# Performance work log

Measured on AMD Instinct MI355X. Metric: run time of the kernel, lower is better.

## Reference

```python
import jax, jax.numpy as jnp
import numpy as np

B, C, D, H, W = 4, 256, 16, 16, 16
REDUCTION = 8
CR = C // REDUCTION  # q/k channel dim = 32


def setup_inputs() -> dict:
    key = jax.random.key(0)
    k1, k2, k3, k4, k5, k6 = jax.random.split(key, 6)
    x = jax.random.normal(k1, (B, C, D, H, W), dtype=jnp.float32)
    # 1x1x1 conv weights are just [out_ch, in_ch] matrices
    Wq = jax.random.normal(k2, (CR, C), dtype=jnp.float32) * (1.0 / np.sqrt(C))
    Wk = jax.random.normal(k3, (CR, C), dtype=jnp.float32) * (1.0 / np.sqrt(C))
    Wv = jax.random.normal(k4, (C, C), dtype=jnp.float32) * (1.0 / np.sqrt(C))
    Wo = jax.random.normal(k5, (C, C), dtype=jnp.float32) * (1.0 / np.sqrt(C))
    gamma = jnp.zeros((1,), dtype=jnp.float32) + 0.5  # nonzero so output depends on attention
    return {"x": x, "Wq": Wq, "Wk": Wk, "Wv": Wv, "Wo": Wo, "gamma": gamma}


def reference(x, Wq, Wk, Wv, Wo, gamma):
    b, c, d, h, w = x.shape
    n = d * h * w
    scale = Wq.shape[0] ** -0.5  # (channels // reduction) ** -0.5
    xf = x.reshape(b, c, n)                      # [B, C, N]
    q = jnp.einsum('oc,bcn->bon', Wq, xf)        # [B, CR, N]
    k = jnp.einsum('oc,bcn->bon', Wk, xf)        # [B, CR, N]
    v = jnp.einsum('oc,bcn->bon', Wv, xf)        # [B, C, N]
    attn = jax.nn.softmax(jnp.einsum('bcn,bcm->bnm', q, k) * scale, axis=-1)  # [B, N, N]
    out = jnp.einsum('bcm,bnm->bcn', v, attn)    # v @ attn^T -> [B, C, N]
    out = jnp.einsum('oc,bcn->bon', Wo, out)     # output 1x1x1 conv
    out = out.reshape(b, c, d, h, w)
    return gamma[0] * out + x
```

## Files before the change

### kernel.cpp

```cpp
#include <hip/hip_runtime.h>
#include <hip/hip_bf16.h>

#define BATCH 4
#define CH 256
#define CRD 32
#define NN 4096

typedef __bf16 bf16x8 __attribute__((ext_vector_type(8)));
typedef float floatx4 __attribute__((ext_vector_type(4)));
typedef float floatx16 __attribute__((ext_vector_type(16)));
typedef unsigned short ushort4v __attribute__((ext_vector_type(4)));
typedef unsigned short ushort8v __attribute__((ext_vector_type(8)));
typedef unsigned int uint2v __attribute__((ext_vector_type(2)));
typedef unsigned int uint4v __attribute__((ext_vector_type(4)));

static __device__ __forceinline__ unsigned short f2bf(float f) {
    __bf16 h = (__bf16)f;
    return __builtin_bit_cast(unsigned short, h);
}
static __device__ __forceinline__ float bf2f(unsigned short h) {
    return __uint_as_float((unsigned int)h << 16);
}


__global__ __launch_bounds__(256) void wconv_kernel(
    const float* __restrict__ Wq, const float* __restrict__ Wk,
    const float* __restrict__ Wv, const float* __restrict__ Wo,
    unsigned short* __restrict__ What, unsigned short* __restrict__ WobF)
{
    const int o = blockIdx.x;
    const int t = threadIdx.x;
    float scale = 1.0f;
    const float* src;
    if (o < 32)      { src = Wq + o * 256;
                       scale = 0.17677669529663687f * 1.4426950408889634f; }
    else if (o < 64) { src = Wk + (o - 32) * 256; }
    else             { src = Wv + (o - 64) * 256; }
    const int mb = o >> 5;
    const size_t idx = ((size_t)(mb * 16 + (t >> 4)) * 64
                        + (o & 31) + 32 * ((t >> 3) & 1)) * 8 + (t & 7);
    What[idx] = f2bf(src[t] * scale);
    if (o < 256) {
        const size_t i2 = ((size_t)((o >> 5) * 16 + (t >> 4)) * 64
                           + (o & 31) + 32 * ((t >> 3) & 1)) * 8 + (t & 7);
        WobF[i2] = f2bf(Wo[o * 256 + t]);
    }
}

static __device__ __forceinline__ uint4v hmerge(
    const ushort4v& xp, const ushort4v& yp, int h)
{
    uint2v xd = __builtin_bit_cast(uint2v, xp);
    uint2v yd = __builtin_bit_cast(uint2v, yp);
    unsigned int px0 = (unsigned int)__shfl_xor((int)xd[0], 32);
    unsigned int px1 = (unsigned int)__shfl_xor((int)xd[1], 32);
    unsigned int py0 = (unsigned int)__shfl_xor((int)yd[0], 32);
    unsigned int py1 = (unsigned int)__shfl_xor((int)yd[1], 32);
    uint4v st;
    st[0] = h ? py0 : xd[0];
    st[1] = h ? py1 : xd[1];
    st[2] = h ? yd[0] : px0;
    st[3] = h ? yd[1] : px1;
    return st;
}

__global__ __launch_bounds__(256, 2) void qkv_kernel(
    const float* __restrict__ x, const unsigned short* __restrict__ What,
    unsigned short* __restrict__ qh, unsigned short* __restrict__ kh,
    unsigned short* __restrict__ vh)
{
    __shared__ __align__(16) unsigned short xf[16 * 512];

    const int t = threadIdx.x;
    const int w = t >> 6;
    const int l = t & 63;
    const int l31 = l & 31;
    const int h = l >> 5;
    const int nt = blockIdx.x, b = blockIdx.y;
    const int n0 = nt * 32;

    {
        const float* xb = x + (size_t)(b * CH) * NN + n0;
        const int n = t & 31;
        const int cq = t >> 5;
        #pragma unroll
        for (int p = 0; p < 8; ++p) {
            int c = p * 32 + cq * 4;
            float v0 = xb[(size_t)(c + 0) * NN + n];
            float v1 = xb[(size_t)(c + 1) * NN + n];
            float v2 = xb[(size_t)(c + 2) * NN + n];
            float v3 = xb[(size_t)(c + 3) * NN + n];
            ushort4v u4;
            u4[0] = f2bf(v0); u4[1] = f2bf(v1); u4[2] = f2bf(v2); u4[3] = f2bf(v3);
            int addr = ((2 * p + (cq >> 2)) * 64 + n + 32 * ((cq >> 1) & 1)) * 8
                       + 4 * (cq & 1);
            *(ushort4v*)&xf[addr] = u4;
        }
    }
    __syncthreads();

    const int mb0 = w, mb1 = w + 4, mb2 = w + 8;
    floatx16 acc0, acc1, acc2;
    #pragma unroll
    for (int i = 0; i < 16; ++i) { acc0[i] = 0.f; acc1[i] = 0.f; acc2[i] = 0.f; }

    for (int kblk = 0; kblk < 16; ++kblk) {
        bf16x8 bf = *(const bf16x8*)&xf[kblk * 512 + l * 8];
        bf16x8 a0 = *(const bf16x8*)(What + ((size_t)(mb0 * 16 + kblk) * 64 + l) * 8);
        bf16x8 a1 = *(const bf16x8*)(What + ((size_t)(mb1 * 16 + kblk) * 64 + l) * 8);
        acc0 = __builtin_amdgcn_mfma_f32_32x32x16_bf16(a0, bf, acc0, 0, 0, 0);
        acc1 = __builtin_amdgcn_mfma_f32_32x32x16_bf16(a1, bf, acc1, 0, 0, 0);
        if (w < 2) {
            bf16x8 a2 = *(const bf16x8*)(What + ((size_t)(mb2 * 16 + kblk) * 64 + l) * 8);
            acc2 = __builtin_amdgcn_mfma_f32_32x32x16_bf16(a2, bf, acc2, 0, 0, 0);
        }
    }

    auto store_qk = [&](unsigned short* dst, const floatx16& a) {
        size_t base = (size_t)(b * 128 + nt) * 1024;
        #pragma unroll
        for (int sb = 0; sb < 2; ++sb) {
            ushort4v xp, yp;
            #pragma unroll
            for (int i = 0; i < 4; ++i) {
                xp[i] = f2bf(a[8 * sb + i]);
                yp[i] = f2bf(a[8 * sb + 4 + i]);
            }
            uint4v st = hmerge(xp, yp, h);
            *(uint4v*)(dst + base + (size_t)sb * 512 + (size_t)l * 8) = st;
        }
    };

    if (w == 0)      store_qk(qh, acc0);
    else if (w == 1) store_qk(kh, acc0);

    __syncthreads();

    auto store_v_lds = [&](int cblk, const floatx16& a) {
        const int chunk = cblk * 2 + (l31 >> 4);
        const int hib = (l31 >> 3) & 1;
        #pragma unroll
        for (int r = 0; r < 16; ++r) {
            int rowo = (r & 3) + 8 * (r >> 2) + 4 * h;
            int unit = chunk * 64 + hib * 32 + rowo;
            int pu = unit ^ ((unit >> 5) & 7);
            xf[pu * 8 + (l31 & 7)] = f2bf(a[r]);
        }
    };

    if (w >= 2) store_v_lds(w - 2, acc0);
    store_v_lds(w + 2, acc1);
    if (w < 2) store_v_lds(w + 6, acc2);

    __syncthreads();

    #pragma unroll
    for (int p = 0; p < 4; ++p) {
        int Lu = p * 256 + t;
        int pu = Lu ^ ((Lu >> 5) & 7);
        uint4v d = *(const uint4v*)&xf[pu * 8];
        int chunk = Lu >> 6;
        int cblk = chunk >> 1, sub = chunk & 1;
        size_t dst = (((size_t)b * 8 + cblk) * 256 + nt * 2 + sub) * 512
                     + (size_t)(Lu & 63) * 8;
        *(uint4v*)(vh + dst) = d;
    }
}

#define SM_M0 12.0f

__global__ __launch_bounds__(256, 4) void attn_kernel(
    const unsigned short* __restrict__ qh, const unsigned short* __restrict__ kh,
    const unsigned short* __restrict__ vh, unsigned short* __restrict__ Opart,
    float* __restrict__ ml)
{
    __shared__ unsigned short p_lds[2 * 8 * 64 * 8];
    __shared__ float psum_s[4][32];

    const int t = threadIdx.x;
    const int w = t >> 6;
    const int l = t & 63;
    const int l31 = l & 31;
    const int h = l >> 5;

    const int lin = blockIdx.x + ((int)blockIdx.y << 7) + ((int)blockIdx.z << 9);
    const int slot = lin >> 3;
    const int combo = ((lin & 7) << 1) | (slot >> 7);
    const int g  = slot & 127;
    const int ks = combo & 3;
    const int b  = combo >> 2;

    const unsigned short* qB = qh + (size_t)(b * 128 + g) * 1024;
    const unsigned short* kB = kh + (size_t)b * 128 * 1024;
    const unsigned short* vB = vh + (size_t)b * 8 * 256 * 512;

    bf16x8 qf0 = *(const bf16x8*)(qB + l * 8);
    bf16x8 qf1 = *(const bf16x8*)(qB + 512 + l * 8);

    bf16x8 kf0 = *(const bf16x8*)(kB + (size_t)(ks * 32 + w) * 1024 + l * 8);
    bf16x8 kf1 = *(const bf16x8*)(kB + (size_t)(ks * 32 + w) * 1024 + 512 + l * 8);

    float l_loc = 0.f;
    floatx16 acc0, acc1;
    #pragma unroll
    for (int i = 0; i < 16; ++i) { acc0[i] = 0.f; acc1[i] = 0.f; }

    for (int it = 0; it < 8; ++it) {
        const int pbase = (it & 1) << 12;

        floatx16 sacc;
        #pragma unroll
        for (int i = 0; i < 16; ++i) sacc[i] = 0.f;
        __builtin_amdgcn_s_setprio(1);
        sacc = __builtin_amdgcn_mfma_f32_32x32x16_bf16(kf0, qf0, sacc, 0, 0, 0);
        sacc = __builtin_amdgcn_mfma_f32_32x32x16_bf16(kf1, qf1, sacc, 0, 0, 0);
        __builtin_amdgcn_s_setprio(0);

        float pv[16];
        #pragma unroll
        for (int r = 0; r < 16; ++r) pv[r] = __builtin_exp2f(sacc[r] - SM_M0);
        float s0 = (pv[0] + pv[1]) + (pv[2] + pv[3]);
        float s1 = (pv[4] + pv[5]) + (pv[6] + pv[7]);
        float s2 = (pv[8] + pv[9]) + (pv[10] + pv[11]);
        float s3 = (pv[12] + pv[13]) + (pv[14] + pv[15]);
        l_loc += (s0 + s1) + (s2 + s3);
        #pragma unroll
        for (int rg = 0; rg < 4; ++rg) {
            ushort4v pk;
            #pragma unroll
            for (int i = 0; i < 4; ++i) pk[i] = f2bf(pv[rg * 4 + i]);
            int idx = pbase
                    + ((2 * w + (rg >> 1)) * 64 + l31 + 32 * (rg & 1)) * 8 + 4 * h;
            *(ushort4v*)&p_lds[idx] = pk;
        }
        if (it < 7) {
            const unsigned short* kn = kB + (size_t)(ks * 32 + (it + 1) * 4 + w) * 1024;
            kf0 = *(const bf16x8*)(kn + l * 8);
            kf1 = *(const bf16x8*)(kn + 512 + l * 8);
        }
        const unsigned short* v0b = vB + ((size_t)(2 * w) * 256 + (ks * 8 + it) * 8) * 512;
        const unsigned short* v1b = vB + ((size_t)(2 * w + 1) * 256 + (ks * 8 + it) * 8) * 512;
        bf16x8 va = *(const bf16x8*)(v0b + l * 8);
        bf16x8 vc = *(const bf16x8*)(v1b + l * 8);

        __syncthreads();

        bf16x8 pf = *(const bf16x8*)&p_lds[pbase + l * 8];
        #pragma unroll
        for (int s = 0; s < 8; ++s) {
            bf16x8 va_n, vc_n, pf_n;
            if (s < 7) {
                va_n = *(const bf16x8*)(v0b + (s + 1) * 512 + l * 8);
                vc_n = *(const bf16x8*)(v1b + (s + 1) * 512 + l * 8);
                pf_n = *(const bf16x8*)&p_lds[pbase + ((s + 1) * 64 + l) * 8];
            }
            __builtin_amdgcn_s_setprio(1);
            acc0 = __builtin_amdgcn_mfma_f32_32x32x16_bf16(va, pf, acc0, 0, 0, 0);
            acc1 = __builtin_amdgcn_mfma_f32_32x32x16_bf16(vc, pf, acc1, 0, 0, 0);
            __builtin_amdgcn_s_setprio(0);
            va = va_n; vc = vc_n; pf = pf_n;
        }
    }

    float lt = l_loc + __shfl_xor(l_loc, 32);
    if (h == 0) psum_s[w][l31] = lt;
    __syncthreads();
    float l_run = (psum_s[0][l31] + psum_s[1][l31])
                + (psum_s[2][l31] + psum_s[3][l31]);

    unsigned short* op = Opart + ((size_t)((b * 128 + g) * 4 + ks)) * 8192;
    #pragma unroll
    for (int ct = 0; ct < 2; ++ct) {
        const floatx16& a = ct ? acc1 : acc0;
        #pragma unroll
        for (int sb = 0; sb < 2; ++sb) {
            ushort4v xp, yp;
            #pragma unroll
            for (int i = 0; i < 4; ++i) {
                xp[i] = f2bf(a[8 * sb + i]);
                yp[i] = f2bf(a[8 * sb + 4 + i]);
            }
            uint4v st = hmerge(xp, yp, h);
            int sP = 4 * w + 2 * ct + sb;
            *(uint4v*)(op + ((size_t)sP * 64 + l) * 8) = st;
        }
    }
    if (w == 0 && h == 0) {
        size_t mb = ((size_t)(b * 128 + g) * 4 + ks) * 64;
        ml[mb + l31] = SM_M0;
        ml[mb + 32 + l31] = l_run;
    }
}

__global__ __launch_bounds__(256, 2) void out_kernel(
    const unsigned short* __restrict__ Opart, const float* __restrict__ ml,
    const unsigned short* __restrict__ WobF, const float* __restrict__ x,
    const float* __restrict__ gamma, float* __restrict__ out)
{
    const int t = threadIdx.x;
    const int w = t >> 6;
    const int l = t & 63;
    const int l31 = l & 31;
    const int h = l >> 5;
    const int qt = blockIdx.x, b = blockIdx.y;

    const size_t slot = (size_t)(b * 128 + qt) * 4;
    float m0 = ml[(slot + 0) * 64 + l31], l0 = ml[(slot + 0) * 64 + 32 + l31];
    float m1 = ml[(slot + 1) * 64 + l31], l1 = ml[(slot + 1) * 64 + 32 + l31];
    float m2 = ml[(slot + 2) * 64 + l31], l2 = ml[(slot + 2) * 64 + 32 + l31];
    float m3 = ml[(slot + 3) * 64 + l31], l3 = ml[(slot + 3) * 64 + 32 + l31];
    float M = fmaxf(fmaxf(m0, m1), fmaxf(m2, m3));
    float e0 = __builtin_exp2f(m0 - M), e1 = __builtin_exp2f(m1 - M);
    float e2 = __builtin_exp2f(m2 - M), e3 = __builtin_exp2f(m3 - M);
    float Lc = l0 * e0 + l1 * e1 + l2 * e2 + l3 * e3;
    float rL = 1.0f / Lc;
    float w0 = e0 * rL, w1 = e1 * rL, w2 = e2 * rL, w3 = e3 * rL;

    const unsigned short* o0 = Opart + (slot + 0) * 8192;
    const unsigned short* o1 = Opart + (slot + 1) * 8192;
    const unsigned short* o2 = Opart + (slot + 2) * 8192;
    const unsigned short* o3 = Opart + (slot + 3) * 8192;

    floatx16 acc[2];
    #pragma unroll
    for (int m = 0; m < 2; ++m)
        #pragma unroll
        for (int i = 0; i < 16; ++i) acc[m][i] = 0.f;

    for (int s = 0; s < 16; ++s) {
        ushort8v f0 = *(const ushort8v*)(o0 + (s * 64 + l) * 8);
        ushort8v f1 = *(const ushort8v*)(o1 + (s * 64 + l) * 8);
        ushort8v f2 = *(const ushort8v*)(o2 + (s * 64 + l) * 8);
        ushort8v f3 = *(const ushort8v*)(o3 + (s * 64 + l) * 8);
        ushort8v cmb;
        #pragma unroll
        for (int j = 0; j < 8; ++j)
            cmb[j] = f2bf(w0 * bf2f(f0[j]) + w1 * bf2f(f1[j])
                        + w2 * bf2f(f2[j]) + w3 * bf2f(f3[j]));
        bf16x8 bfr = *(bf16x8*)&cmb;
        #pragma unroll
        for (int m = 0; m < 2; ++m) {
            int mt = 2 * w + m;
            bf16x8 af = *(const bf16x8*)(WobF + ((size_t)(mt * 16 + s) * 64 + l) * 8);
            acc[m] = __builtin_amdgcn_mfma_f32_32x32x16_bf16(af, bfr, acc[m], 0, 0, 0);
        }
    }

    const float gm = gamma[0];
    #pragma unroll
    for (int m = 0; m < 2; ++m)
        #pragma unroll
        for (int r = 0; r < 16; ++r) {
            int o = (2 * w + m) * 32 + (r & 3) + 8 * (r >> 2) + 4 * h;
            int n = qt * 32 + l31;
            size_t oi = ((size_t)(b * 256 + o)) * NN + n;
            out[oi] = gm * acc[m][r] + x[oi];
        }
}

extern "C" void kernel_launch(void* const* d_in, const int* in_sizes, int n_in,
                              void* d_out, int out_size, void* d_ws, size_t ws_size,
                              hipStream_t stream)
{
    const float* x     = (const float*)d_in[0];
    const float* Wq    = (const float*)d_in[1];
    const float* Wk    = (const float*)d_in[2];
    const float* Wv    = (const float*)d_in[3];
    const float* Wo    = (const float*)d_in[4];
    const float* gamma = (const float*)d_in[5];
    float* out = (float*)d_out;

    char* wsb = (char*)d_ws;
    unsigned short* qh    = (unsigned short*)(wsb);
    unsigned short* kh    = (unsigned short*)(wsb + (1u << 20));
    unsigned short* vh    = (unsigned short*)(wsb + (2u << 20));
    unsigned short* What  = (unsigned short*)(wsb + (10u << 20));
    unsigned short* WobF  = (unsigned short*)(wsb + (10u << 20) + (256u << 10));
    unsigned short* Opart = (unsigned short*)(wsb + (11u << 20));
    float*          ml    = (float*)         (wsb + (45u << 20));

    wconv_kernel<<<320, 256, 0, stream>>>(Wq, Wk, Wv, Wo, What, WobF);

    dim3 g1(128, BATCH);
    qkv_kernel<<<g1, 256, 0, stream>>>(x, What, qh, kh, vh);

    dim3 g2(128, 4, BATCH);
    attn_kernel<<<g2, 256, 0, stream>>>(qh, kh, vh, Opart, ml);

    dim3 g3(128, BATCH);
    out_kernel<<<g3, 256, 0, stream>>>(Opart, ml, WobF, x, gamma, out);
}
```

Baseline: 153.7 us.

## Process two query tiles per attention block to share V loads across tiles

The attention kernel now uses 512 threads per block and covers two 32-row query tiles in each block. Each wave owns a 32-channel slice of V, loads its eight V fragments once, and applies them to the P tiles of both query groups. This halves the number of blocks and the global V traffic per query tile. In exchange, V register pressure per wave rises, LDS use doubles, and the grid shrinks to 1024 blocks, which may reduce latency hiding.

```diff
diff --git a/kernel.cpp b/kernel.cpp
--- a/kernel.cpp
+++ b/kernel.cpp
@@ -169,44 +169,47 @@
 
 #define SM_M0 12.0f
 
-__global__ __launch_bounds__(256, 4) void attn_kernel(
+__global__ __launch_bounds__(512, 4) void attn_kernel(
     const unsigned short* __restrict__ qh, const unsigned short* __restrict__ kh,
     const unsigned short* __restrict__ vh, unsigned short* __restrict__ Opart,
     float* __restrict__ ml)
 {
-    __shared__ unsigned short p_lds[2 * 8 * 64 * 8];
-    __shared__ float psum_s[4][32];
+    __shared__ unsigned short p_lds[2 * 16 * 64 * 8];
+    __shared__ float psum_s[8][32];
 
     const int t = threadIdx.x;
     const int w = t >> 6;
     const int l = t & 63;
     const int l31 = l & 31;
     const int h = l >> 5;
-
-    const int lin = blockIdx.x + ((int)blockIdx.y << 7) + ((int)blockIdx.z << 9);
+    const int wk = w & 3;
+    const int hq = w >> 2;
+
+    const int lin = blockIdx.x + ((int)blockIdx.y << 6) + ((int)blockIdx.z << 8);
     const int slot = lin >> 3;
-    const int combo = ((lin & 7) << 1) | (slot >> 7);
-    const int g  = slot & 127;
+    const int combo = ((lin & 7) << 1) | (slot >> 6);
+    const int gp = slot & 63;
     const int ks = combo & 3;
     const int b  = combo >> 2;
-
-    const unsigned short* qB = qh + (size_t)(b * 128 + g) * 1024;
+    const int g0 = 2 * gp, g1 = 2 * gp + 1;
+
+    const unsigned short* qB = qh + (size_t)(b * 128 + (hq ? g1 : g0)) * 1024;
     const unsigned short* kB = kh + (size_t)b * 128 * 1024;
     const unsigned short* vB = vh + (size_t)b * 8 * 256 * 512;
 
     bf16x8 qf0 = *(const bf16x8*)(qB + l * 8);
     bf16x8 qf1 = *(const bf16x8*)(qB + 512 + l * 8);
 
-    bf16x8 kf0 = *(const bf16x8*)(kB + (size_t)(ks * 32 + w) * 1024 + l * 8);
-    bf16x8 kf1 = *(const bf16x8*)(kB + (size_t)(ks * 32 + w) * 1024 + 512 + l * 8);
+    bf16x8 kf0 = *(const bf16x8*)(kB + (size_t)(ks * 32 + wk) * 1024 + l * 8);
+    bf16x8 kf1 = *(const bf16x8*)(kB + (size_t)(ks * 32 + wk) * 1024 + 512 + l * 8);
 
     float l_loc = 0.f;
-    floatx16 acc0, acc1;
-    #pragma unroll
-    for (int i = 0; i < 16; ++i) { acc0[i] = 0.f; acc1[i] = 0.f; }
+    floatx16 acc_a, acc_b;
+    #pragma unroll
+    for (int i = 0; i < 16; ++i) { acc_a[i] = 0.f; acc_b[i] = 0.f; }
 
     for (int it = 0; it < 8; ++it) {
-        const int pbase = (it & 1) << 12;
+        const int pbase = (it & 1) << 13;
 
         floatx16 sacc;
         #pragma unroll
@@ -230,48 +233,72 @@
             #pragma unroll
             for (int i = 0; i < 4; ++i) pk[i] = f2bf(pv[rg * 4 + i]);
             int idx = pbase
-                    + ((2 * w + (rg >> 1)) * 64 + l31 + 32 * (rg & 1)) * 8 + 4 * h;
+                    + ((hq * 8 + 2 * wk + (rg >> 1)) * 64
+                       + l31 + 32 * (rg & 1)) * 8 + 4 * h;
             *(ushort4v*)&p_lds[idx] = pk;
         }
         if (it < 7) {
-            const unsigned short* kn = kB + (size_t)(ks * 32 + (it + 1) * 4 + w) * 1024;
+            const unsigned short* kn = kB + (size_t)(ks * 32 + (it + 1) * 4 + wk) * 1024;
             kf0 = *(const bf16x8*)(kn + l * 8);
             kf1 = *(const bf16x8*)(kn + 512 + l * 8);
         }
-        const unsigned short* v0b = vB + ((size_t)(2 * w) * 256 + (ks * 8 + it) * 8) * 512;
-        const unsigned short* v1b = vB + ((size_t)(2 * w + 1) * 256 + (ks * 8 + it) * 8) * 512;
-        bf16x8 va = *(const bf16x8*)(v0b + l * 8);
-        bf16x8 vc = *(const bf16x8*)(v1b + l * 8);
+        const unsigned short* v0b = vB + ((size_t)w * 256 + (ks * 8 + it) * 8) * 512;
+        bf16x8 va0 = *(const bf16x8*)(v0b + 0 * 512 + l * 8);
+        bf16x8 va1 = *(const bf16x8*)(v0b + 1 * 512 + l * 8);
+        bf16x8 va2 = *(const bf16x8*)(v0b + 2 * 512 + l * 8);
+        bf16x8 va3 = *(const bf16x8*)(v0b + 3 * 512 + l * 8);
+        bf16x8 va4 = *(const bf16x8*)(v0b + 4 * 512 + l * 8);
+        bf16x8 va5 = *(const bf16x8*)(v0b + 5 * 512 + l * 8);
+        bf16x8 va6 = *(const bf16x8*)(v0b + 6 * 512 + l * 8);
+        bf16x8 va7 = *(const bf16x8*)(v0b + 7 * 512 + l * 8);
 
         __syncthreads();
 
-        bf16x8 pf = *(const bf16x8*)&p_lds[pbase + l * 8];
+        bf16x8 pa = *(const bf16x8*)&p_lds[pbase + l * 8];
+        bf16x8 pb = *(const bf16x8*)&p_lds[pbase + 4096 + l * 8];
         #pragma unroll
         for (int s = 0; s < 8; ++s) {
-            bf16x8 va_n, vc_n, pf_n;
+            bf16x8 vcur = (s == 0) ? va0 : (s == 1) ? va1 : (s == 2) ? va2
+                        : (s == 3) ? va3 : (s == 4) ? va4 : (s == 5) ? va5
+                        : (s == 6) ? va6 : va7;
+            bf16x8 pa_n, pb_n;
             if (s < 7) {
-                va_n = *(const bf16x8*)(v0b + (s + 1) * 512 + l * 8);
-                vc_n = *(const bf16x8*)(v1b + (s + 1) * 512 + l * 8);
-                pf_n = *(const bf16x8*)&p_lds[pbase + ((s + 1) * 64 + l) * 8];
+                pa_n = *(const bf16x8*)&p_lds[pbase + ((s + 1) * 64 + l) * 8];
+                pb_n = *(const bf16x8*)&p_lds[pbase + 4096 + ((s + 1) * 64 + l) * 8];
             }
             __builtin_amdgcn_s_setprio(1);
-            acc0 = __builtin_amdgcn_mfma_f32_32x32x16_bf16(va, pf, acc0, 0, 0, 0);
-            acc1 = __builtin_amdgcn_mfma_f32_32x32x16_bf16(vc, pf, acc1, 0, 0, 0);
+            acc_a = __builtin_amdgcn_mfma_f32_32x32x16_bf16(vcur, pa, acc_a, 0, 0, 0);
+            acc_b = __builtin_amdgcn_mfma_f32_32x32x16_bf16(vcur, pb, acc_b, 0, 0, 0);
             __builtin_amdgcn_s_setprio(0);
-            va = va_n; vc = vc_n; pf = pf_n;
+            pa = pa_n; pb = pb_n;
         }
     }
 
     float lt = l_loc + __shfl_xor(l_loc, 32);
     if (h == 0) psum_s[w][l31] = lt;
     __syncthreads();
-    float l_run = (psum_s[0][l31] + psum_s[1][l31])
-                + (psum_s[2][l31] + psum_s[3][l31]);
-
-    unsigned short* op = Opart + ((size_t)((b * 128 + g) * 4 + ks)) * 8192;
+
+    if (w == 0 && h == 0) {
+        float l_run = (psum_s[0][l31] + psum_s[1][l31])
+                    + (psum_s[2][l31] + psum_s[3][l31]);
+        size_t mb = ((size_t)(b * 128 + g0) * 4 + ks) * 64;
+        ml[mb + l31] = SM_M0;
+        ml[mb + 32 + l31] = l_run;
+    }
+    if (w == 4 && h == 0) {
+        float l_run = (psum_s[4][l31] + psum_s[5][l31])
+                    + (psum_s[6][l31] + psum_s[7][l31]);
+        size_t mb = ((size_t)(b * 128 + g1) * 4 + ks) * 64;
+        ml[mb + l31] = SM_M0;
+        ml[mb + 32 + l31] = l_run;
+    }
+
+    unsigned short* opa = Opart + ((size_t)((b * 128 + g0) * 4 + ks)) * 8192;
+    unsigned short* opb = Opart + ((size_t)((b * 128 + g1) * 4 + ks)) * 8192;
     #pragma unroll
     for (int ct = 0; ct < 2; ++ct) {
-        const floatx16& a = ct ? acc1 : acc0;
+        const floatx16& a = ct ? acc_b : acc_a;
+        unsigned short* op = ct ? opb : opa;
         #pragma unroll
         for (int sb = 0; sb < 2; ++sb) {
             ushort4v xp, yp;
@@ -281,14 +308,9 @@
                 yp[i] = f2bf(a[8 * sb + 4 + i]);
             }
             uint4v st = hmerge(xp, yp, h);
-            int sP = 4 * w + 2 * ct + sb;
+            int sP = 2 * w + sb;
             *(uint4v*)(op + ((size_t)sP * 64 + l) * 8) = st;
         }
-    }
-    if (w == 0 && h == 0) {
-        size_t mb = ((size_t)(b * 128 + g) * 4 + ks) * 64;
-        ml[mb + l31] = SM_M0;
-        ml[mb + 32 + l31] = l_run;
     }
 }
 
@@ -384,8 +406,8 @@
     dim3 g1(128, BATCH);
     qkv_kernel<<<g1, 256, 0, stream>>>(x, What, qh, kh, vh);
 
-    dim3 g2(128, 4, BATCH);
-    attn_kernel<<<g2, 256, 0, stream>>>(qh, kh, vh, Opart, ml);
+    dim3 g2(64, 4, BATCH);
+    attn_kernel<<<g2, 512, 0, stream>>>(qh, kh, vh, Opart, ml);
 
     dim3 g3(128, BATCH);
     out_kernel<<<g3, 256, 0, stream>>>(Opart, ml, WobF, x, gamma, out);
```

New measurement: 149.5 us. 1.03x faster.
